# Kernel optimization log

Hardware: AMD Instinct MI355X
Metric: run time of the kernel (lower is better)

## Reference

```python
import jax, jax.numpy as jnp
import numpy as np

B, V, H, NI, E = 512, 50, 768, 8, 2


def setup_inputs() -> dict:
    key = jax.random.key(0)
    ks = jax.random.split(key, 8)
    s1 = 1.0 / np.sqrt(2 * H)
    s = 1.0 / np.sqrt(H)
    return {
        "variable_states": jax.random.normal(ks[0], (B, V, H), jnp.float32),
        "edge_probs": jax.random.uniform(ks[1], (B, V, V, E), jnp.float32),
        "intervention_values": jax.random.normal(ks[2], (B, NI, H), jnp.float32),
        "W1": jax.random.normal(ks[3], (2 * H, H), jnp.float32) * s1,
        "b1": jnp.zeros((H,), jnp.float32),
        "W2": jax.random.normal(ks[4], (H, H), jnp.float32) * s,
        "b2": jnp.zeros((H,), jnp.float32),
        "Wg1": jax.random.normal(ks[5], (H, H), jnp.float32) * s,
        "bg1": jnp.zeros((H,), jnp.float32),
        "Wg2": jax.random.normal(ks[6], (H, 1), jnp.float32) * s,
        "bg2": jnp.zeros((1,), jnp.float32),
        "intervention_indices": jax.random.randint(ks[7], (B, NI), 0, V, jnp.int64),
    }


def _do_operator(variable_states, intervention_values, intervention_indices,
                 W1, b1, W2, b2, Wg1, bg1, Wg2, bg2):
    idx = intervention_indices                              # [B, NI]
    valid = (idx >= 0) & (idx < V)                          # [B, NI]
    idx_c = jnp.clip(idx, 0, V - 1)
    # gather all original vars for every intervention at once: [B, NI, H]
    orig = jnp.take_along_axis(variable_states, idx_c[..., None], axis=1)
    x = jnp.concatenate([orig, intervention_values], axis=-1)      # [B, NI, 2H]
    enc = jax.nn.gelu(x @ W1 + b1, approximate=False) @ W2 + b2    # [B, NI, H]
    gate = jax.nn.sigmoid(
        jax.nn.gelu(enc @ Wg1 + bg1, approximate=False) @ Wg2 + bg2
    )                                                              # [B, NI, 1]
    blended = orig * (1.0 - gate) + intervention_values * gate     # [B, NI, H]
    states = variable_states
    b_ar = jnp.arange(B)
    for i in range(NI):
        cur = states[b_ar, idx_c[:, i]]                            # [B, H]
        new = jnp.where(valid[:, i, None], blended[:, i], cur)
        states = states.at[b_ar, idx_c[:, i]].set(new)
    return states


def reference(variable_states, edge_probs, intervention_values,
              W1, b1, W2, b2, Wg1, bg1, Wg2, bg2, intervention_indices):
    # edge_probs is mutated in-place in the torch original but not returned;
    # the returned value is only the intervened states.
    return _do_operator(variable_states, intervention_values, intervention_indices,
                        W1, b1, W2, b2, Wg1, bg1, Wg2, bg2)
```

## Files before the change

kernel.cpp:

```cpp
#include <hip/hip_runtime.h>
#include <math.h>

#define B_  512
#define V_  50
#define H_  768
#define NI_ 8
#define M_  (B_ * NI_)
#define K1_ (2 * H_)
#define NCB_ 12
#define N4_     4915200
#define SPLIT4_ 2949120

using f32x4 = __attribute__((ext_vector_type(4))) float;
using s16x8 = __attribute__((ext_vector_type(8))) short;

__device__ __forceinline__ float gelu_exact(float x) {
    return 0.5f * x * (1.0f + erff(x * 0.7071067811865476f));
}

__device__ __forceinline__ short f2bf(float f) {
    union { float f; unsigned u; } v; v.f = f;
    unsigned r = (v.u + 0x7fffu + ((v.u >> 16) & 1u)) >> 16;
    return (short)r;
}

#define GLOAD16(g, l)                                                          \
    __builtin_amdgcn_global_load_lds(                                          \
        (const __attribute__((address_space(1))) void*)(g),                    \
        (__attribute__((address_space(3))) void*)(l), 16, 0, 0)

__device__ __forceinline__ short* lds_ptr(short* base, int row, int byteoff) {
    return (short*)((char*)base + row * 128 + (byteoff ^ ((row & 7) << 4)));
}

__global__ __launch_bounds__(256) void pre_kernel(
    const float* __restrict__ vs, const float* __restrict__ iv,
    const int* __restrict__ idx,
    const float* __restrict__ W1, const float* __restrict__ W2,
    const float* __restrict__ Wg1,
    const float* __restrict__ b2, const float* __restrict__ bg1,
    short* __restrict__ W1t, short* __restrict__ W2b, short* __restrict__ Wg1t,
    short* __restrict__ X, float* __restrict__ bc) {
    __shared__ short s[64][65];
    const int blk = blockIdx.x;
    const int tid = threadIdx.x;

    if (blk < 288 || (blk >= 432 && blk < 576)) {
        const float* src; short* dst; int K, t;
        if (blk < 288) { src = W1;  dst = W1t;  K = K1_; t = blk; }
        else           { src = Wg1; dst = Wg1t; K = H_;  t = blk - 432; }
        int bx = t % 12, by = t / 12;
        int k0 = by * 64, n0 = bx * 64;
#pragma unroll
        for (int e = 0; e < 16; ++e) {
            int li = tid + e * 256;
            int kk = li >> 6, nn = li & 63;
            s[kk][nn] = f2bf(src[(size_t)(k0 + kk) * H_ + n0 + nn]);
        }
        __syncthreads();
#pragma unroll
        for (int e = 0; e < 16; ++e) {
            int li = tid + e * 256;
            int nn = li >> 6, kk = li & 63;
            dst[(size_t)(n0 + nn) * K + k0 + kk] = s[kk][nn];
        }
    } else if (blk < 432) {
        size_t base = (size_t)(blk - 288) * 4096;
#pragma unroll
        for (int e = 0; e < 4; ++e) {
            size_t i = base + (size_t)e * 1024 + tid * 4;
            float4 a = *(const float4*)(W2 + i);
            short4 o;
            o.x = f2bf(a.x); o.y = f2bf(a.y); o.z = f2bf(a.z); o.w = f2bf(a.w);
            *(short4*)(W2b + i) = o;
        }
    } else if (blk < 1600) {
        int g = blk - 576;
        int r = g * 4 + (tid >> 6);
        int lane = tid & 63;
        int b = r >> 3;
        int id = idx[r];
        id = min(max(id, 0), V_ - 1);
        const float4* s1 = (const float4*)(vs + ((size_t)b * V_ + id) * H_);
        const float4* s2 = (const float4*)(iv + (size_t)r * H_);
        short* xr = X + (size_t)r * K1_;
#pragma unroll
        for (int part = 0; part < 3; ++part) {
            int e = lane + part * 64;
            float4 a = s1[e];
            float4 c = s2[e];
            short4 oa, oc;
            oa.x = f2bf(a.x); oa.y = f2bf(a.y); oa.z = f2bf(a.z); oa.w = f2bf(a.w);
            oc.x = f2bf(c.x); oc.y = f2bf(c.y); oc.z = f2bf(c.z); oc.w = f2bf(c.w);
            *(short4*)&xr[e * 4] = oa;
            *(short4*)&xr[H_ + e * 4] = oc;
        }
    } else {
        __shared__ float part[4][64];
        int c = blk - 1600;
        int sub = tid >> 6;
        int jj = tid & 63;
        int j = c * 64 + jj;
        float sum = 0.f;
        for (int k = sub * 192; k < sub * 192 + 192; ++k)
            sum += b2[k] * Wg1[(size_t)k * H_ + j];
        part[sub][jj] = sum;
        __syncthreads();
        if (sub == 0)
            bc[j] = part[0][jj] + part[1][jj] + part[2][jj] + part[3][jj] + bg1[j];
    }
}

__device__ __forceinline__ void gemm_body(
    const short* __restrict__ A, const short* __restrict__ Bt,
    const float* __restrict__ bias, short* __restrict__ C,
    int N, int K, int act, int row0, int col0,
    short (*As)[128 * 64], short (*Bs)[64 * 64], int tid) {
    const int lane = tid & 63;
    const int wave = tid >> 6;
    const int llo = lane & 15;
    const int lhi = lane >> 4;

    const short* gsrc[6];
    short* ldst0[6];
    int lstep[6];
#pragma unroll
    for (int p = 0; p < 6; ++p) {
        int c = wave * 6 + p;
        int jj = lane & 7;
        if (c < 16) {
            int r = c * 8 + (lane >> 3);
            int j = jj ^ (r & 7);
            gsrc[p] = A + (size_t)(row0 + r) * K + j * 8;
            ldst0[p] = &As[0][c * 512];
            lstep[p] = 128 * 64;
        } else {
            int r = (c - 16) * 8 + (lane >> 3);
            int j = jj ^ (r & 7);
            gsrc[p] = Bt + (size_t)(col0 + r) * K + j * 8;
            ldst0[p] = &Bs[0][(c - 16) * 512];
            lstep[p] = 64 * 64;
        }
    }

    f32x4 acc[2][4];
#pragma unroll
    for (int mi = 0; mi < 2; ++mi)
#pragma unroll
        for (int nf = 0; nf < 4; ++nf) acc[mi][nf] = (f32x4){0, 0, 0, 0};

    const int nt = K >> 6;
#pragma unroll
    for (int p = 0; p < 6; ++p) GLOAD16(gsrc[p], ldst0[p]);
    __syncthreads();

    for (int t = 0; t < nt; ++t) {
        const int cur = t & 1;
        if (t + 1 < nt) {
#pragma unroll
            for (int p = 0; p < 6; ++p)
                GLOAD16(gsrc[p] + (size_t)(t + 1) * 64,
                        ldst0[p] + (cur ^ 1) * lstep[p]);
        }
        short* Ab = (short*)As[cur];
        short* Bb = (short*)Bs[cur];
#pragma unroll
        for (int ks = 0; ks < 2; ++ks) {
            s16x8 a[2], b[4];
#pragma unroll
            for (int mi = 0; mi < 2; ++mi)
                a[mi] = *(const s16x8*)lds_ptr(Ab, wave * 32 + mi * 16 + llo,
                                               ks * 64 + lhi * 16);
#pragma unroll
            for (int nf = 0; nf < 4; ++nf)
                b[nf] = *(const s16x8*)lds_ptr(Bb, nf * 16 + llo,
                                               ks * 64 + lhi * 16);
#pragma unroll
            for (int mi = 0; mi < 2; ++mi)
#pragma unroll
                for (int nf = 0; nf < 4; ++nf)
                    acc[mi][nf] = __builtin_amdgcn_mfma_f32_16x16x32_bf16(
                        a[mi], b[nf], acc[mi][nf], 0, 0, 0);
        }
        __syncthreads();
    }

#pragma unroll
    for (int nf = 0; nf < 4; ++nf) {
        int cc = col0 + nf * 16 + llo;
        float bv = bias ? bias[cc] : 0.0f;
#pragma unroll
        for (int mi = 0; mi < 2; ++mi) {
#pragma unroll
            for (int j = 0; j < 4; ++j) {
                int rr = row0 + wave * 32 + mi * 16 + lhi * 4 + j;
                float v = acc[mi][nf][j] + bv;
                if (act) v = gelu_exact(v);
                C[(size_t)rr * N + cc] = f2bf(v);
            }
        }
    }
}

__global__ __launch_bounds__(256) void mega1(
    const short* __restrict__ Xb, const short* __restrict__ W1t,
    const float* __restrict__ b1, short* __restrict__ h1b,
    const short* __restrict__ Wg1t, const short* __restrict__ W2b,
    short* __restrict__ Wct,
    const float4* __restrict__ cs, float4* __restrict__ cd) {
    __shared__ short As[2][128 * 64];
    __shared__ short Bs[2][64 * 64];
    const int bid = blockIdx.x;
    const int tid = threadIdx.x;

    if (bid < 384) {
        int sw = (bid & 7) * 48 + (bid >> 3);
        int bx = sw % 12, by = sw / 12;
        gemm_body(Xb, W1t, b1, h1b, H_, K1_, 1, by * 128, bx * 64, As, Bs, tid);
    } else if (bid < 456) {
        int t = bid - 384;
        int bx = t % 12, by = t / 12;
        gemm_body(Wg1t, W2b, nullptr, Wct, H_, H_, 0, by * 128, bx * 64, As, Bs, tid);
    } else {
        int lb = bid - 456;
        for (size_t i = (size_t)lb * 256 + tid; i < (size_t)SPLIT4_;
             i += (size_t)184 * 256)
            cd[i] = cs[i];
    }
}

__global__ __launch_bounds__(256) void gate_gemm(
    const short* __restrict__ h1b, const short* __restrict__ Wct,
    const float* __restrict__ bc, const float* __restrict__ wg2,
    float* __restrict__ gate_part,
    const float4* __restrict__ cs, float4* __restrict__ cd) {
    __shared__ short As[2][128 * 64];
    __shared__ short Bs[2][64 * 64];
    const int bid = blockIdx.x;
    const int tid = threadIdx.x;

    if (bid >= 384) {
        int lb = bid - 384;
        for (size_t i = (size_t)SPLIT4_ + (size_t)lb * 256 + tid; i < (size_t)N4_;
             i += (size_t)256 * 256)
            cd[i] = cs[i];
        return;
    }

    const int lane = tid & 63;
    const int wave = tid >> 6;
    const int llo = lane & 15;
    const int lhi = lane >> 4;
    int sw = (bid & 7) * 48 + (bid >> 3);
    int bx = sw % 12, by = sw / 12;
    const int row0 = by * 128;
    const int col0 = bx * 64;
    const int K = H_;

    const short* gsrc[6];
    short* ldst0[6];
    int lstep[6];
#pragma unroll
    for (int p = 0; p < 6; ++p) {
        int c = wave * 6 + p;
        int jj = lane & 7;
        if (c < 16) {
            int r = c * 8 + (lane >> 3);
            int j = jj ^ (r & 7);
            gsrc[p] = h1b + (size_t)(row0 + r) * K + j * 8;
            ldst0[p] = &As[0][c * 512];
            lstep[p] = 128 * 64;
        } else {
            int r = (c - 16) * 8 + (lane >> 3);
            int j = jj ^ (r & 7);
            gsrc[p] = Wct + (size_t)(col0 + r) * K + j * 8;
            ldst0[p] = &Bs[0][(c - 16) * 512];
            lstep[p] = 64 * 64;
        }
    }

    f32x4 acc[2][4];
#pragma unroll
    for (int mi = 0; mi < 2; ++mi)
#pragma unroll
        for (int nf = 0; nf < 4; ++nf) acc[mi][nf] = (f32x4){0, 0, 0, 0};

    const int nt = K >> 6;
#pragma unroll
    for (int p = 0; p < 6; ++p) GLOAD16(gsrc[p], ldst0[p]);
    __syncthreads();

    for (int t = 0; t < nt; ++t) {
        const int cur = t & 1;
        if (t + 1 < nt) {
#pragma unroll
            for (int p = 0; p < 6; ++p)
                GLOAD16(gsrc[p] + (size_t)(t + 1) * 64,
                        ldst0[p] + (cur ^ 1) * lstep[p]);
        }
        short* Ab = (short*)As[cur];
        short* Bb = (short*)Bs[cur];
#pragma unroll
        for (int ks = 0; ks < 2; ++ks) {
            s16x8 a[2], b[4];
#pragma unroll
            for (int mi = 0; mi < 2; ++mi)
                a[mi] = *(const s16x8*)lds_ptr(Ab, wave * 32 + mi * 16 + llo,
                                               ks * 64 + lhi * 16);
#pragma unroll
            for (int nf = 0; nf < 4; ++nf)
                b[nf] = *(const s16x8*)lds_ptr(Bb, nf * 16 + llo,
                                               ks * 64 + lhi * 16);
#pragma unroll
            for (int mi = 0; mi < 2; ++mi)
#pragma unroll
                for (int nf = 0; nf < 4; ++nf)
                    acc[mi][nf] = __builtin_amdgcn_mfma_f32_16x16x32_bf16(
                        a[mi], b[nf], acc[mi][nf], 0, 0, 0);
        }
        __syncthreads();
    }

    float s[2][4];
#pragma unroll
    for (int mi = 0; mi < 2; ++mi)
#pragma unroll
        for (int j = 0; j < 4; ++j) s[mi][j] = 0.f;
#pragma unroll
    for (int nf = 0; nf < 4; ++nf) {
        int cc = col0 + nf * 16 + llo;
        float bv = bc[cc];
        float wv = wg2[cc];
#pragma unroll
        for (int mi = 0; mi < 2; ++mi)
#pragma unroll
            for (int j = 0; j < 4; ++j)
                s[mi][j] += gelu_exact(acc[mi][nf][j] + bv) * wv;
    }
#pragma unroll
    for (int off = 1; off < 16; off <<= 1)
#pragma unroll
        for (int mi = 0; mi < 2; ++mi)
#pragma unroll
            for (int j = 0; j < 4; ++j)
                s[mi][j] += __shfl_xor(s[mi][j], off);
    if (llo == 0) {
#pragma unroll
        for (int mi = 0; mi < 2; ++mi)
#pragma unroll
            for (int j = 0; j < 4; ++j) {
                int rr = row0 + wave * 32 + mi * 16 + lhi * 4 + j;
                gate_part[(size_t)rr * NCB_ + bx] = s[mi][j];
            }
    }
}

__global__ __launch_bounds__(192) void final_blend(
    const float* __restrict__ vs, const float* __restrict__ iv,
    const int* __restrict__ idx, const float* __restrict__ gate_part,
    const float* __restrict__ bg2, float* __restrict__ out) {
    int r = blockIdx.x;
    int b = r >> 3, i = r & 7;
    int id = idx[r];
    if (id < 0 || id >= V_) return;
    for (int j = i + 1; j < NI_; ++j)
        if (idx[b * NI_ + j] == id) return;
    __shared__ float gsh;
    if (threadIdx.x == 0) {
        float s = bg2[0];
#pragma unroll
        for (int c = 0; c < NCB_; ++c) s += gate_part[(size_t)r * NCB_ + c];
        gsh = 1.f / (1.f + expf(-s));
    }
    __syncthreads();
    float g = gsh;
    int t = threadIdx.x;
    const float4* src = (const float4*)(vs + ((size_t)b * V_ + id) * H_);
    const float4* ivr = (const float4*)(iv + (size_t)r * H_);
    float4* dst = (float4*)(out + ((size_t)b * V_ + id) * H_);
    float4 o = src[t], x = ivr[t], res;
    res.x = o.x * (1.f - g) + x.x * g;
    res.y = o.y * (1.f - g) + x.y * g;
    res.z = o.z * (1.f - g) + x.z * g;
    res.w = o.w * (1.f - g) + x.w * g;
    dst[t] = res;
}

extern "C" void kernel_launch(void* const* d_in, const int* in_sizes, int n_in,
                              void* d_out, int out_size, void* d_ws, size_t ws_size,
                              hipStream_t stream) {
    const float* vs  = (const float*)d_in[0];
    const float* iv  = (const float*)d_in[2];
    const float* W1  = (const float*)d_in[3];
    const float* b1  = (const float*)d_in[4];
    const float* W2  = (const float*)d_in[5];
    const float* b2  = (const float*)d_in[6];
    const float* Wg1 = (const float*)d_in[7];
    const float* bg1 = (const float*)d_in[8];
    const float* Wg2 = (const float*)d_in[9];
    const float* bg2 = (const float*)d_in[10];
    const int*   idx = (const int*)d_in[11];
    float* out = (float*)d_out;

    char* ws = (char*)d_ws;
    short* Xb   = (short*)ws;
    short* h1b  = (short*)(ws + (size_t)M_ * K1_ * 2);
    float* gate_part = (float*)(ws + (size_t)M_ * K1_ * 2 + (size_t)M_ * H_ * 2);
    short* W1t  = (short*)((char*)gate_part + (size_t)M_ * NCB_ * 4);
    short* W2b  = W1t + (size_t)H_ * K1_;
    short* Wg1t = W2b + (size_t)H_ * H_;
    short* Wct  = Wg1t + (size_t)H_ * H_;
    float* bc   = (float*)(Wct + (size_t)H_ * H_);

    const float4* cs = (const float4*)vs;
    float4* cd = (float4*)out;

    pre_kernel<<<1612, 256, 0, stream>>>(vs, iv, idx, W1, W2, Wg1, b2, bg1,
                                         W1t, W2b, Wg1t, Xb, bc);
    mega1<<<640, 256, 0, stream>>>(Xb, W1t, b1, h1b, Wg1t, W2b, Wct, cs, cd);
    gate_gemm<<<640, 256, 0, stream>>>(h1b, Wct, bc, Wg2, gate_part, cs, cd);
    final_blend<<<M_, 192, 0, stream>>>(vs, iv, idx, gate_part, bg2, out);
}
```

Baseline: 75.44 us.

## Single-buffer GEMM LDS for higher occupancy and rebalance unrolled copy blocks

Both GEMM kernels drop the double-buffered LDS tiles in favour of a single buffer that is loaded and synchronised each k-step, and now declare launch bounds of 6 blocks per CU. The aim is to raise occupancy so that other resident waves hide load latency. The output copy of variable_states is spread over many more blocks, each doing a 10-load unrolled batch, with the split between the two kernels moved. This gives up the in-block prefetch overlap, so performance now relies on other waves filling the stall during each k-step.

```diff
diff --git a/kernel.cpp b/kernel.cpp
--- a/kernel.cpp
+++ b/kernel.cpp
@@ -9,7 +9,9 @@
 #define K1_ (2 * H_)
 #define NCB_ 12
 #define N4_     4915200
-#define SPLIT4_ 2949120
+#define SPLIT4_ 2764800
+#define CPB1_   1080
+#define CPB2_   840
 
 using f32x4 = __attribute__((ext_vector_type(4))) float;
 using s16x8 = __attribute__((ext_vector_type(8))) short;
@@ -111,19 +113,36 @@
     }
 }
 
+template <int NBLK>
+__device__ __forceinline__ void copy2x5(const float4* __restrict__ cs,
+                                        float4* __restrict__ cd,
+                                        size_t start, int lb, int tid) {
+    const size_t step = (size_t)NBLK * 256;
+    size_t base = start + (size_t)lb * 256 + tid;
+#pragma unroll
+    for (int o = 0; o < 2; ++o) {
+        float4 t[5];
+#pragma unroll
+        for (int u = 0; u < 5; ++u)
+            t[u] = cs[base + (size_t)(o * 5 + u) * step];
+#pragma unroll
+        for (int u = 0; u < 5; ++u)
+            cd[base + (size_t)(o * 5 + u) * step] = t[u];
+    }
+}
+
 __device__ __forceinline__ void gemm_body(
     const short* __restrict__ A, const short* __restrict__ Bt,
     const float* __restrict__ bias, short* __restrict__ C,
     int N, int K, int act, int row0, int col0,
-    short (*As)[128 * 64], short (*Bs)[64 * 64], int tid) {
+    short* As, short* Bs, int tid) {
     const int lane = tid & 63;
     const int wave = tid >> 6;
     const int llo = lane & 15;
     const int lhi = lane >> 4;
 
     const short* gsrc[6];
-    short* ldst0[6];
-    int lstep[6];
+    short* ldst[6];
 #pragma unroll
     for (int p = 0; p < 6; ++p) {
         int c = wave * 6 + p;
@@ -132,14 +151,12 @@
             int r = c * 8 + (lane >> 3);
             int j = jj ^ (r & 7);
             gsrc[p] = A + (size_t)(row0 + r) * K + j * 8;
-            ldst0[p] = &As[0][c * 512];
-            lstep[p] = 128 * 64;
+            ldst[p] = As + c * 512 + (lane & 7) * 8 + (lane >> 3) * 64;
         } else {
             int r = (c - 16) * 8 + (lane >> 3);
             int j = jj ^ (r & 7);
             gsrc[p] = Bt + (size_t)(col0 + r) * K + j * 8;
-            ldst0[p] = &Bs[0][(c - 16) * 512];
-            lstep[p] = 64 * 64;
+            ldst[p] = Bs + (c - 16) * 512 + (lane & 7) * 8 + (lane >> 3) * 64;
         }
     }
 
@@ -150,30 +167,22 @@
         for (int nf = 0; nf < 4; ++nf) acc[mi][nf] = (f32x4){0, 0, 0, 0};
 
     const int nt = K >> 6;
-#pragma unroll
-    for (int p = 0; p < 6; ++p) GLOAD16(gsrc[p], ldst0[p]);
-    __syncthreads();
-
     for (int t = 0; t < nt; ++t) {
-        const int cur = t & 1;
-        if (t + 1 < nt) {
-#pragma unroll
-            for (int p = 0; p < 6; ++p)
-                GLOAD16(gsrc[p] + (size_t)(t + 1) * 64,
-                        ldst0[p] + (cur ^ 1) * lstep[p]);
-        }
-        short* Ab = (short*)As[cur];
-        short* Bb = (short*)Bs[cur];
+#pragma unroll
+        for (int p = 0; p < 6; ++p)
+            GLOAD16(gsrc[p] + (size_t)t * 64, ldst[p]);
+        __syncthreads();
+
 #pragma unroll
         for (int ks = 0; ks < 2; ++ks) {
             s16x8 a[2], b[4];
 #pragma unroll
             for (int mi = 0; mi < 2; ++mi)
-                a[mi] = *(const s16x8*)lds_ptr(Ab, wave * 32 + mi * 16 + llo,
+                a[mi] = *(const s16x8*)lds_ptr(As, wave * 32 + mi * 16 + llo,
                                                ks * 64 + lhi * 16);
 #pragma unroll
             for (int nf = 0; nf < 4; ++nf)
-                b[nf] = *(const s16x8*)lds_ptr(Bb, nf * 16 + llo,
+                b[nf] = *(const s16x8*)lds_ptr(Bs, nf * 16 + llo,
                                                ks * 64 + lhi * 16);
 #pragma unroll
             for (int mi = 0; mi < 2; ++mi)
@@ -202,14 +211,14 @@
     }
 }
 
-__global__ __launch_bounds__(256) void mega1(
+__global__ __launch_bounds__(256, 6) void mega1(
     const short* __restrict__ Xb, const short* __restrict__ W1t,
     const float* __restrict__ b1, short* __restrict__ h1b,
     const short* __restrict__ Wg1t, const short* __restrict__ W2b,
     short* __restrict__ Wct,
     const float4* __restrict__ cs, float4* __restrict__ cd) {
-    __shared__ short As[2][128 * 64];
-    __shared__ short Bs[2][64 * 64];
+    __shared__ short As[128 * 64];
+    __shared__ short Bs[64 * 64];
     const int bid = blockIdx.x;
     const int tid = threadIdx.x;
 
@@ -222,28 +231,22 @@
         int bx = t % 12, by = t / 12;
         gemm_body(Wg1t, W2b, nullptr, Wct, H_, H_, 0, by * 128, bx * 64, As, Bs, tid);
     } else {
-        int lb = bid - 456;
-        for (size_t i = (size_t)lb * 256 + tid; i < (size_t)SPLIT4_;
-             i += (size_t)184 * 256)
-            cd[i] = cs[i];
-    }
-}
-
-__global__ __launch_bounds__(256) void gate_gemm(
+        copy2x5<CPB1_>(cs, cd, 0, bid - 456, tid);
+    }
+}
+
+__global__ __launch_bounds__(256, 6) void gate_gemm(
     const short* __restrict__ h1b, const short* __restrict__ Wct,
     const float* __restrict__ bc, const float* __restrict__ wg2,
     float* __restrict__ gate_part,
     const float4* __restrict__ cs, float4* __restrict__ cd) {
-    __shared__ short As[2][128 * 64];
-    __shared__ short Bs[2][64 * 64];
+    __shared__ short As[128 * 64];
+    __shared__ short Bs[64 * 64];
     const int bid = blockIdx.x;
     const int tid = threadIdx.x;
 
     if (bid >= 384) {
-        int lb = bid - 384;
-        for (size_t i = (size_t)SPLIT4_ + (size_t)lb * 256 + tid; i < (size_t)N4_;
-             i += (size_t)256 * 256)
-            cd[i] = cs[i];
+        copy2x5<CPB2_>(cs, cd, SPLIT4_, bid - 384, tid);
         return;
     }
 
@@ -258,8 +261,7 @@
     const int K = H_;
 
     const short* gsrc[6];
-    short* ldst0[6];
-    int lstep[6];
+    short* ldst[6];
 #pragma unroll
     for (int p = 0; p < 6; ++p) {
         int c = wave * 6 + p;
@@ -268,14 +270,12 @@
             int r = c * 8 + (lane >> 3);
             int j = jj ^ (r & 7);
             gsrc[p] = h1b + (size_t)(row0 + r) * K + j * 8;
-            ldst0[p] = &As[0][c * 512];
-            lstep[p] = 128 * 64;
+            ldst[p] = As + c * 512 + (lane & 7) * 8 + (lane >> 3) * 64;
         } else {
             int r = (c - 16) * 8 + (lane >> 3);
             int j = jj ^ (r & 7);
             gsrc[p] = Wct + (size_t)(col0 + r) * K + j * 8;
-            ldst0[p] = &Bs[0][(c - 16) * 512];
-            lstep[p] = 64 * 64;
+            ldst[p] = Bs + (c - 16) * 512 + (lane & 7) * 8 + (lane >> 3) * 64;
         }
     }
 
@@ -286,30 +286,22 @@
         for (int nf = 0; nf < 4; ++nf) acc[mi][nf] = (f32x4){0, 0, 0, 0};
 
     const int nt = K >> 6;
-#pragma unroll
-    for (int p = 0; p < 6; ++p) GLOAD16(gsrc[p], ldst0[p]);
-    __syncthreads();
-
     for (int t = 0; t < nt; ++t) {
-        const int cur = t & 1;
-        if (t + 1 < nt) {
-#pragma unroll
-            for (int p = 0; p < 6; ++p)
-                GLOAD16(gsrc[p] + (size_t)(t + 1) * 64,
-                        ldst0[p] + (cur ^ 1) * lstep[p]);
-        }
-        short* Ab = (short*)As[cur];
-        short* Bb = (short*)Bs[cur];
+#pragma unroll
+        for (int p = 0; p < 6; ++p)
+            GLOAD16(gsrc[p] + (size_t)t * 64, ldst[p]);
+        __syncthreads();
+
 #pragma unroll
         for (int ks = 0; ks < 2; ++ks) {
             s16x8 a[2], b[4];
 #pragma unroll
             for (int mi = 0; mi < 2; ++mi)
-                a[mi] = *(const s16x8*)lds_ptr(Ab, wave * 32 + mi * 16 + llo,
+                a[mi] = *(const s16x8*)lds_ptr(As, wave * 32 + mi * 16 + llo,
                                                ks * 64 + lhi * 16);
 #pragma unroll
             for (int nf = 0; nf < 4; ++nf)
-                b[nf] = *(const s16x8*)lds_ptr(Bb, nf * 16 + llo,
+                b[nf] = *(const s16x8*)lds_ptr(Bs, nf * 16 + llo,
                                                ks * 64 + lhi * 16);
 #pragma unroll
             for (int mi = 0; mi < 2; ++mi)
@@ -417,7 +409,7 @@
 
     pre_kernel<<<1612, 256, 0, stream>>>(vs, iv, idx, W1, W2, Wg1, b2, bg1,
                                          W1t, W2b, Wg1t, Xb, bc);
-    mega1<<<640, 256, 0, stream>>>(Xb, W1t, b1, h1b, Wg1t, W2b, Wct, cs, cd);
-    gate_gemm<<<640, 256, 0, stream>>>(h1b, Wct, bc, Wg2, gate_part, cs, cd);
+    mega1<<<1536, 256, 0, stream>>>(Xb, W1t, b1, h1b, Wg1t, W2b, Wct, cs, cd);
+    gate_gemm<<<1224, 256, 0, stream>>>(h1b, Wct, bc, Wg2, gate_part, cs, cd);
     final_blend<<<M_, 192, 0, stream>>>(vs, iv, idx, gate_part, bg2, out);
 }
```

New measurement: 104.4 us. 1.38x slower.
